# Kernel optimization log

Hardware: AMD Instinct MI355X
Metric: run time of the kernel (lower is better)

## Reference

```python
import jax, jax.numpy as jnp
import numpy as np

B, S, D, H = 2, 2048, 1024, 16
DK = D // H

def setup_inputs() -> dict:
    key = jax.random.key(0)
    ks = jax.random.split(key, 11)
    s = 1.0 / np.sqrt(D)
    return {
        "q": jax.random.normal(ks[0], (B, S, D), jnp.float32),
        "k": jax.random.normal(ks[1], (B, S, D), jnp.float32),
        "v": jax.random.normal(ks[2], (B, S, D), jnp.float32),
        "Wq": jax.random.normal(ks[3], (D, D), jnp.float32) * s,
        "bq": jax.random.normal(ks[4], (D,), jnp.float32) * s,
        "Wk": jax.random.normal(ks[5], (D, D), jnp.float32) * s,
        "bk": jax.random.normal(ks[6], (D,), jnp.float32) * s,
        "Wv": jax.random.normal(ks[7], (D, D), jnp.float32) * s,
        "bv": jax.random.normal(ks[8], (D,), jnp.float32) * s,
        "Wo": jax.random.normal(ks[9], (D, D), jnp.float32) * s,
        "bo": jax.random.normal(ks[10], (D,), jnp.float32) * s,
    }

def reference(q, k, v, Wq, bq, Wk, bk, Wv, bv, Wo, bo):
    # Linear projections, then split into heads: [B,S,D] -> [B,H,S,DK]
    def heads(x, W, b):
        y = x @ W.T + b
        return y.reshape(B, S, H, DK).transpose(0, 2, 1, 3)
    qh = heads(q, Wq, bq)
    kh = heads(k, Wk, bk)
    vh = heads(v, Wv, bv)
    scores = jnp.einsum('bhsd,bhtd->bhst', qh, kh) / jnp.sqrt(jnp.float32(DK))
    attn = jax.nn.softmax(scores, axis=-1)
    out = jnp.einsum('bhst,bhtd->bhsd', attn, vh)  # [B,H,S,DK]
    out = out.transpose(0, 2, 1, 3).reshape(B, S, D)
    return out @ Wo.T + bo
```

## Files before the change

kernel.cpp:

```cpp
#include <hip/hip_runtime.h>
#include <stdint.h>

#define B_  2
#define S_  2048
#define D_  1024
#define H_  16
#define DK_ 64

typedef unsigned short u16;
typedef __attribute__((ext_vector_type(8))) __bf16 bf16x8;
typedef __attribute__((ext_vector_type(4))) float f32x4;
typedef __attribute__((ext_vector_type(16))) float f32x16;
typedef __attribute__((ext_vector_type(4))) short short4v;
typedef __attribute__((ext_vector_type(8))) short short8v;

static __device__ __forceinline__ u16 f2bf(float f) {
    union { float f; uint32_t u; } v; v.f = f;
    return (u16)((v.u + 0x7fffu + ((v.u >> 16) & 1u)) >> 16);
}
static __device__ __forceinline__ uint32_t pk2bf(float x, float y) {
    return (uint32_t)f2bf(x) | ((uint32_t)f2bf(y) << 16);
}
static __device__ __forceinline__ uint32_t cvtpk_bf16(float lo, float hi) {
    uint32_t r; asm("v_cvt_pk_bf16_f32 %0, %1, %2" : "=v"(r) : "v"(lo), "v"(hi));
    return r;
}
static __device__ __forceinline__ float exp2f_fast(float x) {
    float r; asm("v_exp_f32 %0, %1" : "=v"(r) : "v"(x)); return r;
}

#define GLOAD16(gp, lp) \
    __builtin_amdgcn_global_load_lds((const __attribute__((address_space(1))) void*)(gp), \
                                     (__attribute__((address_space(3))) void*)(lp), 16, 0, 0)

static __device__ __forceinline__ int swz(int lin) { return lin ^ ((lin >> 3) & 7); }

static __device__ __forceinline__ int xcd_swz(int bid, int cpx) {
    return (bid & 7) * cpx + (bid >> 3);
}

__global__ __launch_bounds__(256) void cast_all_kernel(
        const float* __restrict__ q, const float* __restrict__ k, const float* __restrict__ v,
        const float* __restrict__ Wq, const float* __restrict__ Wk,
        const float* __restrict__ Wv, const float* __restrict__ Wo,
        u16* __restrict__ qb, u16* __restrict__ kb, u16* __restrict__ vb,
        u16* __restrict__ Wqb, u16* __restrict__ Wkb, u16* __restrict__ Wvb,
        u16* __restrict__ Wob) {
    int blk = blockIdx.x;
    const float* src; u16* dst; int off;
    if (blk < 2048)      { src = q;  dst = qb;  off = blk; }
    else if (blk < 4096) { src = k;  dst = kb;  off = blk - 2048; }
    else if (blk < 6144) { src = v;  dst = vb;  off = blk - 4096; }
    else if (blk < 6656) { src = Wq; dst = Wqb; off = blk - 6144; }
    else if (blk < 7168) { src = Wk; dst = Wkb; off = blk - 6656; }
    else if (blk < 7680) { src = Wv; dst = Wvb; off = blk - 7168; }
    else                 { src = Wo; dst = Wob; off = blk - 7680; }
    int i = (off * 256 + threadIdx.x) * 8;
    float4 a = *(const float4*)(src + i);
    float4 b = *(const float4*)(src + i + 4);
    uint4 r;
    r.x = pk2bf(a.x, a.y); r.y = pk2bf(a.z, a.w);
    r.z = pk2bf(b.x, b.y); r.w = pk2bf(b.z, b.w);
    *(uint4*)(void*)(dst + i) = r;
}

__device__ __forceinline__ void gemm128_compute(
        const u16* __restrict__ X, const u16* __restrict__ W,
        int m0, int n0, u16* lds, f32x4 acc[4][4]) {
    const int tid = threadIdx.x, lane = tid & 63, w = tid >> 6;
    const int wm = w >> 1, wn = w & 1;
    u16* As = lds;
    u16* Bs = lds + 8192;

    auto stage = [&](int bi, int kt) {
#pragma unroll
        for (int r = 0; r < 2; ++r) {
            int s = tid + (r << 8);
            int lin = s ^ ((s >> 3) & 7);
            int row = lin >> 2, ch = lin & 3;
            GLOAD16(X + (size_t)(m0 + row) * 1024 + (kt << 5) + (ch << 3),
                    (char*)(As + bi * 4096) + ((r << 8) + (w << 6)) * 16);
            GLOAD16(W + (size_t)(n0 + row) * 1024 + (kt << 5) + (ch << 3),
                    (char*)(Bs + bi * 4096) + ((r << 8) + (w << 6)) * 16);
        }
    };

    stage(0, 0);
    asm volatile("s_waitcnt vmcnt(0)" ::: "memory");
    __syncthreads();
#pragma unroll 1
    for (int kt = 0; kt < 32; ++kt) {
        const int cur = kt & 1;
        if (kt < 31) stage(cur ^ 1, kt + 1);
        const char* Ab = (const char*)(As + cur * 4096);
        const char* Bb = (const char*)(Bs + cur * 4096);
        bf16x8 a[4], b[4];
#pragma unroll
        for (int f = 0; f < 4; ++f) {
            int rowa = wm * 64 + f * 16 + (lane & 15);
            a[f] = *(const bf16x8*)(Ab + swz(rowa * 4 + (lane >> 4)) * 16);
            int rowb = wn * 64 + f * 16 + (lane & 15);
            b[f] = *(const bf16x8*)(Bb + swz(rowb * 4 + (lane >> 4)) * 16);
        }
#pragma unroll
        for (int fm = 0; fm < 4; ++fm)
#pragma unroll
            for (int fn = 0; fn < 4; ++fn)
                acc[fm][fn] = __builtin_amdgcn_mfma_f32_16x16x32_bf16(
                    a[fm], b[fn], acc[fm][fn], 0, 0, 0);
        __syncthreads();
    }
}

__device__ __forceinline__ void stage_half(const u16* __restrict__ src,
        int R0, int kt, u16* dst, int tid) {
#pragma unroll
    for (int r = 0; r < 2; ++r) {
        int s = tid + (r << 9);
        int lin = s ^ ((s >> 3) & 7);
        int row = lin >> 3, ch = lin & 7;
        GLOAD16(src + (size_t)(R0 + row) * 1024 + (kt << 6) + (ch << 3),
                (char*)dst + ((r << 9) + ((tid >> 6) << 6)) * 16);
    }
}

#define VM4  asm volatile("s_waitcnt vmcnt(4)" ::: "memory")
#define VM0  asm volatile("s_waitcnt vmcnt(0)" ::: "memory")

#define PHASE(QQ, MP, LOADB, STAGE_STMT, VM_STMT)                                \
    {                                                                            \
        bf16x8 afr[2][2];                                                        \
        if (LOADB) {                                                             \
            _Pragma("unroll") for (int fn = 0; fn < 4; ++fn)                     \
            _Pragma("unroll") for (int ks = 0; ks < 2; ++ks) {                   \
                int lin = (brow0 + fn * 16 + (lane & 15)) * 8 + ks * 4 + (lane >> 4); \
                bfr[fn][ks] = *(const bf16x8*)(Bhb[QQ] + swz(lin) * 16);         \
            }                                                                    \
        }                                                                        \
        _Pragma("unroll") for (int fo = 0; fo < 2; ++fo)                         \
        _Pragma("unroll") for (int ks = 0; ks < 2; ++ks) {                       \
            int lin = ((MP) * 32 + fo * 16 + (lane & 15)) * 8 + ks * 4 + (lane >> 4); \
            afr[fo][ks] = *(const bf16x8*)(Ahb[QQ] + swz(lin) * 16);             \
        }                                                                        \
        STAGE_STMT;                                                              \
        VM_STMT;                                                                 \
        __builtin_amdgcn_s_barrier();                                            \
        __builtin_amdgcn_sched_barrier(0);                                       \
        __builtin_amdgcn_s_setprio(1);                                           \
        _Pragma("unroll") for (int fo = 0; fo < 2; ++fo)                         \
        _Pragma("unroll") for (int ks = 0; ks < 2; ++ks)                         \
        _Pragma("unroll") for (int fn = 0; fn < 4; ++fn)                         \
            acc[(MP) * 2 + fo][fn] = __builtin_amdgcn_mfma_f32_16x16x32_bf16(    \
                afr[fo][ks], bfr[fn][ks], acc[(MP) * 2 + fo][fn], 0, 0, 0);      \
        __builtin_amdgcn_s_setprio(0);                                           \
        __builtin_amdgcn_s_barrier();                                            \
        __builtin_amdgcn_sched_barrier(0);                                       \
    }

__global__ __launch_bounds__(512, 2) void qkv256_kernel(
        const u16* __restrict__ qX, const u16* __restrict__ kX, const u16* __restrict__ vX,
        const u16* __restrict__ Wq, const u16* __restrict__ Wk, const u16* __restrict__ Wv,
        const float* __restrict__ bq, const float* __restrict__ bk, const float* __restrict__ bv,
        u16* __restrict__ qo, u16* __restrict__ ko, u16* __restrict__ vt) {
    __shared__ __align__(16) u16 lds[65536];
    const int tid = threadIdx.x, lane = tid & 63, w = tid >> 6;
    const int wm = w >> 2, wn = w & 3;
    const int lg = xcd_swz(blockIdx.x, 24);
    const int which = lg >> 6;
    const int rem = lg & 63;
    const int n0 = (rem >> 4) << 8;
    const int m0 = (rem & 15) << 8;
    const u16* X = which == 0 ? qX : (which == 1 ? kX : vX);
    const u16* W = which == 0 ? Wq : (which == 1 ? Wk : Wv);
    const float* bias = which == 0 ? bq : (which == 1 ? bk : bv);

    u16* Abase = lds;
    u16* Bbase = lds + 32768;

    stage_half(X, m0,        0, Abase + 0,             tid);
    stage_half(X, m0 + 128,  0, Abase + 8192,          tid);
    stage_half(W, n0,        0, Bbase + 0,             tid);
    stage_half(W, n0 + 128,  0, Bbase + 8192,          tid);
    stage_half(W, n0,        1, Bbase + 16384,         tid);
    stage_half(W, n0 + 128,  1, Bbase + 16384 + 8192,  tid);
    VM4;
    __builtin_amdgcn_s_barrier();
    __builtin_amdgcn_sched_barrier(0);

    f32x4 acc[8][4] = {};
    bf16x8 bfr[4][2];
    const char* Ahb[2] = { (const char*)(Abase + wm * 8192),
                           (const char*)(Abase + 16384 + wm * 8192) };
    const char* Bhb[2] = { (const char*)(Bbase + (wn >> 1) * 8192),
                           (const char*)(Bbase + 16384 + (wn >> 1) * 8192) };
    const int brow0 = (wn & 1) * 64;

#pragma unroll 1
    for (int i = 0; i < 8; ++i) {
        const int t0 = 2 * i, t1 = 2 * i + 1;
        const bool nl = (i < 7);
        PHASE(0, 0, true,  stage_half(X, m0,       t1,     Abase + 16384,        tid), (void)0);
        PHASE(0, 1, false, stage_half(X, m0 + 128, t1,     Abase + 16384 + 8192, tid), (void)0);
        PHASE(0, 2, false, if (nl) stage_half(W, n0,       t0 + 2, Bbase + 0,    tid), (void)0);
        PHASE(0, 3, false, if (nl) stage_half(W, n0 + 128, t0 + 2, Bbase + 8192, tid),
              if (nl) { VM4; } else { VM0; });
        PHASE(1, 0, true,  if (nl) stage_half(X, m0,       t0 + 2, Abase + 0,    tid), (void)0);
        PHASE(1, 1, false, if (nl) stage_half(X, m0 + 128, t0 + 2, Abase + 8192, tid), (void)0);
        PHASE(1, 2, false, if (nl) stage_half(W, n0,       t1 + 2, Bbase + 16384, tid), (void)0);
        PHASE(1, 3, false, if (nl) stage_half(W, n0 + 128, t1 + 2, Bbase + 16384 + 8192, tid),
              if (nl) { VM4; });
    }

    if (which < 2) {
        u16* out = which == 0 ? qo : ko;
        const float scale = which == 0 ? 0.1803368801111883f : 1.0f;
#pragma unroll
        for (int fn = 0; fn < 4; ++fn) {
            int n = n0 + wn * 64 + fn * 16 + (lane & 15);
            float bb = bias[n];
            int h = n >> 6, dk = n & 63;
#pragma unroll
            for (int fm = 0; fm < 8; ++fm)
#pragma unroll
                for (int j = 0; j < 4; ++j) {
                    int m = m0 + wm * 128 + fm * 16 + (lane >> 4) * 4 + j;
                    int b = m >> 11, s = m & 2047;
                    out[((size_t)(b * H_ + h) * S_ + s) * DK_ + dk] =
                        f2bf((acc[fm][fn][j] + bb) * scale);
                }
        }
    } else {
        __syncthreads();
        u16* wl = lds + w * 8192;
#pragma unroll
        for (int fn = 0; fn < 4; ++fn) {
            int dk = fn * 16 + (lane & 15);
            float bb = bias[n0 + wn * 64 + dk];
            int xr = (dk & 7) << 3;
#pragma unroll
            for (int fm = 0; fm < 8; ++fm) {
                int sl = fm * 16 + (lane >> 4) * 4;
                short4v p;
#pragma unroll
                for (int j = 0; j < 4; ++j) p[j] = (short)f2bf(acc[fm][fn][j] + bb);
                *(short4v*)(void*)&wl[dk * 128 + (sl ^ xr)] = p;
            }
        }
        int mrow = m0 + wm * 128;
        int b = mrow >> 11, sbase = mrow & 2047;
        int h = (n0 >> 6) + wn;
        u16* dst = vt + ((size_t)(b * H_ + h) * DK_) * S_ + sbase;
#pragma unroll
        for (int oc = 0; oc < 8; ++oc)
#pragma unroll
            for (int ic = 0; ic < 2; ++ic) {
                int dk = oc * 8 + (lane >> 3);
                int sc = ic * 8 + (lane & 7);
                short8v vv = *(const short8v*)(const void*)
                    &wl[dk * 128 + ((sc * 8) ^ ((dk & 7) << 3))];
                *(short8v*)(void*)(dst + (size_t)dk * S_ + sc * 8) = vv;
            }
    }
}

__global__ __launch_bounds__(256) void oproj_kernel(
        const u16* __restrict__ X, const u16* __restrict__ W,
        const float* __restrict__ bias, float* __restrict__ out) {
    __shared__ __align__(16) u16 lds[16384];
    const int bid = xcd_swz(blockIdx.x, 32);
    const int m0 = (bid >> 3) << 7;
    const int n0 = (bid & 7) << 7;
    f32x4 acc[4][4] = {};
    gemm128_compute(X, W, m0, n0, lds, acc);

    const int lane = threadIdx.x & 63, w = threadIdx.x >> 6;
    const int wm = w >> 1, wn = w & 1;
#pragma unroll
    for (int fn = 0; fn < 4; ++fn) {
        int n = n0 + wn * 64 + fn * 16 + (lane & 15);
        float bb = bias[n];
#pragma unroll
        for (int fm = 0; fm < 4; ++fm)
#pragma unroll
            for (int j = 0; j < 4; ++j) {
                int m = m0 + wm * 64 + fm * 16 + (lane >> 4) * 4 + j;
                out[(size_t)m * 1024 + n] = acc[fm][fn][j] + bb;
            }
    }
}

__global__ __launch_bounds__(256, 2) void attn_kernel(
        const u16* __restrict__ qh, const u16* __restrict__ kh,
        const u16* __restrict__ Vt, u16* __restrict__ ao) {
    __shared__ __align__(16) u16 Qs[8192];
    __shared__ __align__(16) u16 Ks[2][4096];
    __shared__ __align__(16) u16 Vs[2][4096];

    const int tid = threadIdx.x, lane = tid & 63, w = tid >> 6;
    const int l31 = lane & 31, hh = lane >> 5;
    const int lg = xcd_swz(blockIdx.x, 64);
    const int bh = lg >> 4, qt = lg & 15;
    const u16* qg = qh + ((size_t)bh * S_ + qt * 128) * DK_;
    const u16* kg = kh + (size_t)bh * S_ * DK_;
    const u16* vg = Vt + (size_t)bh * DK_ * S_;

    auto stageKV = [&](int bi, int kt) {
#pragma unroll
        for (int r = 0; r < 2; ++r) {
            int s = tid + (r << 8);
            int lin = s ^ ((s >> 3) & 7);
            int row = lin >> 3, ch = lin & 7;
            GLOAD16(kg + (size_t)(kt * 64 + row) * 64 + (ch << 3),
                    (char*)(&Ks[bi][0]) + ((r << 8) + (w << 6)) * 16);
            GLOAD16(vg + (size_t)row * S_ + kt * 64 + (ch << 3),
                    (char*)(&Vs[bi][0]) + ((r << 8) + (w << 6)) * 16);
        }
    };

#pragma unroll
    for (int r = 0; r < 4; ++r) {
        int s = tid + (r << 8);
        int lin = s ^ ((s >> 3) & 7);
        int row = lin >> 3, ch = lin & 7;
        GLOAD16(qg + row * 64 + (ch << 3), (char*)Qs + ((r << 8) + (w << 6)) * 16);
    }
    stageKV(0, 0);
    asm volatile("s_waitcnt vmcnt(0)" ::: "memory");
    __syncthreads();

    bf16x8 qf[4];
#pragma unroll
    for (int c = 0; c < 4; ++c) {
        int row = w * 32 + l31;
        qf[c] = *(const bf16x8*)((const char*)Qs + swz(row * 8 + c * 2 + hh) * 16);
    }

    union { short8v s; bf16x8 b; } onesu;
#pragma unroll
    for (int i = 0; i < 8; ++i) onesu.s[i] = 0x3F80;
    const bf16x8 onesf = onesu.b;

    f32x16 acc[2] = {};
    f32x16 accl = {};

#pragma unroll 1
    for (int kt = 0; kt < 32; ++kt) {
        const int cur = kt & 1;
        if (kt < 31) stageKV(cur ^ 1, kt + 1);
        const char* Kb = (const char*)&Ks[cur][0];
        const char* Vb = (const char*)&Vs[cur][0];

        f32x16 st[2] = {};
#pragma unroll
        for (int kb = 0; kb < 2; ++kb) {
            bf16x8 kf[4];
#pragma unroll
            for (int c = 0; c < 4; ++c) {
                int row = kb * 32 + l31;
                kf[c] = *(const bf16x8*)(Kb + swz(row * 8 + c * 2 + hh) * 16);
            }
            __builtin_amdgcn_s_setprio(1);
#pragma unroll
            for (int c = 0; c < 4; ++c)
                st[kb] = __builtin_amdgcn_mfma_f32_32x32x16_bf16(
                    kf[c], qf[c], st[kb], 0, 0, 0);
            __builtin_amdgcn_s_setprio(0);
        }

        bf16x8 pa[4];
#pragma unroll
        for (int c = 0; c < 4; ++c) {
            const int kb = c >> 1, o = (c & 1) * 8;
            float e0 = exp2f_fast(st[kb][o + 0]);
            float e1 = exp2f_fast(st[kb][o + 1]);
            float e2 = exp2f_fast(st[kb][o + 2]);
            float e3 = exp2f_fast(st[kb][o + 3]);
            float e4 = exp2f_fast(st[kb][o + 4]);
            float e5 = exp2f_fast(st[kb][o + 5]);
            float e6 = exp2f_fast(st[kb][o + 6]);
            float e7 = exp2f_fast(st[kb][o + 7]);
            uint32_t u0 = cvtpk_bf16(e0, e1);
            uint32_t u1 = cvtpk_bf16(e2, e3);
            uint32_t u2 = cvtpk_bf16(e4, e5);
            uint32_t u3 = cvtpk_bf16(e6, e7);
            asm volatile("v_permlane32_swap_b32 %0, %1" : "+v"(u0), "+v"(u2));
            asm volatile("v_permlane32_swap_b32 %0, %1" : "+v"(u1), "+v"(u3));
            union { uint32_t u[4]; bf16x8 v; } pu;
            pu.u[0] = u0; pu.u[1] = u1; pu.u[2] = u2; pu.u[3] = u3;
            pa[c] = pu.v;
        }

        __builtin_amdgcn_s_setprio(1);
#pragma unroll
        for (int c = 0; c < 4; ++c)
            accl = __builtin_amdgcn_mfma_f32_32x32x16_bf16(
                pa[c], onesf, accl, 0, 0, 0);
        __builtin_amdgcn_s_setprio(0);
#pragma unroll
        for (int nb = 0; nb < 2; ++nb) {
            bf16x8 vf[4];
#pragma unroll
            for (int c = 0; c < 4; ++c) {
                int row = nb * 32 + l31;
                vf[c] = *(const bf16x8*)(Vb + swz(row * 8 + c * 2 + hh) * 16);
            }
            __builtin_amdgcn_s_setprio(1);
#pragma unroll
            for (int c = 0; c < 4; ++c)
                acc[nb] = __builtin_amdgcn_mfma_f32_32x32x16_bf16(
                    pa[c], vf[c], acc[nb], 0, 0, 0);
            __builtin_amdgcn_s_setprio(0);
        }
        __syncthreads();
    }

    const int bb = bh >> 4, hd = bh & 15;
#pragma unroll
    for (int r = 0; r < 16; ++r) {
        float inv = 1.0f / accl[r];
        int ql = (r & 3) + 8 * (r >> 2) + 4 * hh;
        int srow = qt * 128 + w * 32 + ql;
#pragma unroll
        for (int nb = 0; nb < 2; ++nb) {
            int col = hd * 64 + nb * 32 + l31;
            ao[((size_t)bb * S_ + srow) * D_ + col] = f2bf(acc[nb][r] * inv);
        }
    }
}

extern "C" void kernel_launch(void* const* d_in, const int* in_sizes, int n_in,
                              void* d_out, int out_size, void* d_ws, size_t ws_size,
                              hipStream_t stream) {
    const float* q  = (const float*)d_in[0];
    const float* k  = (const float*)d_in[1];
    const float* v  = (const float*)d_in[2];
    const float* Wq = (const float*)d_in[3];
    const float* bq = (const float*)d_in[4];
    const float* Wk = (const float*)d_in[5];
    const float* bk = (const float*)d_in[6];
    const float* Wv = (const float*)d_in[7];
    const float* bv = (const float*)d_in[8];
    const float* Wo = (const float*)d_in[9];
    const float* bo = (const float*)d_in[10];

    char* ws = (char*)d_ws;
    u16* qb  = (u16*)(ws);
    u16* kb  = (u16*)(ws + (8u  << 20));
    u16* vb  = (u16*)(ws + (16u << 20));
    u16* Wqb = (u16*)(ws + (24u << 20));
    u16* Wkb = (u16*)(ws + (26u << 20));
    u16* Wvb = (u16*)(ws + (28u << 20));
    u16* Wob = (u16*)(ws + (30u << 20));
    u16* qhb = (u16*)(ws + (32u << 20));
    u16* khb = (u16*)(ws + (40u << 20));
    u16* Vtb = (u16*)(ws + (48u << 20));
    u16* aob = kb;

    cast_all_kernel<<<8192, 256, 0, stream>>>(q, k, v, Wq, Wk, Wv, Wo,
                                              qb, kb, vb, Wqb, Wkb, Wvb, Wob);

    qkv256_kernel<<<192, 512, 0, stream>>>(
        qb, kb, vb, Wqb, Wkb, Wvb, bq, bk, bv, qhb, khb, Vtb);

    attn_kernel<<<512, 256, 0, stream>>>(qhb, khb, Vtb, aob);

    oproj_kernel<<<256, 256, 0, stream>>>(aob, Wob, bo, (float*)d_out);
}
```

Baseline: 117.1 us.

## Process two KV tiles per barrier with 4-slot staging and VALU rowsum

The attention loop now handles two 64-key tiles per iteration, using a 4-slot LDS ring that prefetches two tiles ahead, so barriers are halved. The softmax denominator is accumulated with VALU adds and a cross-lane shuffle instead of an extra MFMA against a ones matrix. The swizzle gains an extra XOR term to change LDS bank mapping. LDS use doubles (about 80KB per block), which may reduce occupancy relative to the launch bound of 2 blocks per CU.

```diff
diff --git a/kernel.cpp b/kernel.cpp
--- a/kernel.cpp
+++ b/kernel.cpp
@@ -34,6 +34,9 @@
                                      (__attribute__((address_space(3))) void*)(lp), 16, 0, 0)
 
 static __device__ __forceinline__ int swz(int lin) { return lin ^ ((lin >> 3) & 7); }
+static __device__ __forceinline__ int swz2(int lin) {
+    return lin ^ ((lin >> 3) & 7) ^ ((lin >> 6) & 3);
+}
 
 static __device__ __forceinline__ int xcd_swz(int bid, int cpx) {
     return (bid & 7) * cpx + (bid >> 3);
@@ -293,8 +296,8 @@
         const u16* __restrict__ qh, const u16* __restrict__ kh,
         const u16* __restrict__ Vt, u16* __restrict__ ao) {
     __shared__ __align__(16) u16 Qs[8192];
-    __shared__ __align__(16) u16 Ks[2][4096];
-    __shared__ __align__(16) u16 Vs[2][4096];
+    __shared__ __align__(16) u16 Ks[4][4096];
+    __shared__ __align__(16) u16 Vs[4][4096];
 
     const int tid = threadIdx.x, lane = tid & 63, w = tid >> 6;
     const int l31 = lane & 31, hh = lane >> 5;
@@ -304,27 +307,28 @@
     const u16* kg = kh + (size_t)bh * S_ * DK_;
     const u16* vg = Vt + (size_t)bh * DK_ * S_;
 
-    auto stageKV = [&](int bi, int kt) {
+    auto stageKV = [&](int slot, int kt) {
 #pragma unroll
         for (int r = 0; r < 2; ++r) {
             int s = tid + (r << 8);
-            int lin = s ^ ((s >> 3) & 7);
+            int lin = swz2(s);
             int row = lin >> 3, ch = lin & 7;
             GLOAD16(kg + (size_t)(kt * 64 + row) * 64 + (ch << 3),
-                    (char*)(&Ks[bi][0]) + ((r << 8) + (w << 6)) * 16);
+                    (char*)(&Ks[slot][0]) + ((r << 8) + (w << 6)) * 16);
             GLOAD16(vg + (size_t)row * S_ + kt * 64 + (ch << 3),
-                    (char*)(&Vs[bi][0]) + ((r << 8) + (w << 6)) * 16);
+                    (char*)(&Vs[slot][0]) + ((r << 8) + (w << 6)) * 16);
         }
     };
 
 #pragma unroll
     for (int r = 0; r < 4; ++r) {
         int s = tid + (r << 8);
-        int lin = s ^ ((s >> 3) & 7);
+        int lin = swz2(s);
         int row = lin >> 3, ch = lin & 7;
         GLOAD16(qg + row * 64 + (ch << 3), (char*)Qs + ((r << 8) + (w << 6)) * 16);
     }
     stageKV(0, 0);
+    stageKV(1, 1);
     asm volatile("s_waitcnt vmcnt(0)" ::: "memory");
     __syncthreads();
 
@@ -332,93 +336,84 @@
 #pragma unroll
     for (int c = 0; c < 4; ++c) {
         int row = w * 32 + l31;
-        qf[c] = *(const bf16x8*)((const char*)Qs + swz(row * 8 + c * 2 + hh) * 16);
-    }
-
-    union { short8v s; bf16x8 b; } onesu;
-#pragma unroll
-    for (int i = 0; i < 8; ++i) onesu.s[i] = 0x3F80;
-    const bf16x8 onesf = onesu.b;
+        qf[c] = *(const bf16x8*)((const char*)Qs + swz2(row * 8 + c * 2 + hh) * 16);
+    }
 
     f32x16 acc[2] = {};
-    f32x16 accl = {};
+    float rs = 0.f;
+
+#define ATTN_TILE(SLOT, PAOUT)                                                   \
+    {                                                                            \
+        const char* Kb = (const char*)&Ks[SLOT][0];                              \
+        f32x16 st[2] = {};                                                       \
+        _Pragma("unroll") for (int kb = 0; kb < 2; ++kb) {                       \
+            bf16x8 kf[4];                                                        \
+            _Pragma("unroll") for (int c = 0; c < 4; ++c) {                      \
+                int row = kb * 32 + l31;                                         \
+                kf[c] = *(const bf16x8*)(Kb + swz2(row * 8 + c * 2 + hh) * 16);  \
+            }                                                                    \
+            __builtin_amdgcn_s_setprio(1);                                       \
+            _Pragma("unroll") for (int c = 0; c < 4; ++c)                        \
+                st[kb] = __builtin_amdgcn_mfma_f32_32x32x16_bf16(                \
+                    kf[c], qf[c], st[kb], 0, 0, 0);                              \
+            __builtin_amdgcn_s_setprio(0);                                       \
+        }                                                                        \
+        _Pragma("unroll") for (int c = 0; c < 4; ++c) {                          \
+            const int kb = c >> 1, o = (c & 1) * 8;                              \
+            float e0 = exp2f_fast(st[kb][o + 0]);                                \
+            float e1 = exp2f_fast(st[kb][o + 1]);                                \
+            float e2 = exp2f_fast(st[kb][o + 2]);                                \
+            float e3 = exp2f_fast(st[kb][o + 3]);                                \
+            float e4 = exp2f_fast(st[kb][o + 4]);                                \
+            float e5 = exp2f_fast(st[kb][o + 5]);                                \
+            float e6 = exp2f_fast(st[kb][o + 6]);                                \
+            float e7 = exp2f_fast(st[kb][o + 7]);                                \
+            rs += ((e0 + e1) + (e2 + e3)) + ((e4 + e5) + (e6 + e7));             \
+            uint32_t u0 = cvtpk_bf16(e0, e1);                                    \
+            uint32_t u1 = cvtpk_bf16(e2, e3);                                    \
+            uint32_t u2 = cvtpk_bf16(e4, e5);                                    \
+            uint32_t u3 = cvtpk_bf16(e6, e7);                                    \
+            asm volatile("v_permlane32_swap_b32 %0, %1" : "+v"(u0), "+v"(u2));   \
+            asm volatile("v_permlane32_swap_b32 %0, %1" : "+v"(u1), "+v"(u3));   \
+            union { uint32_t u[4]; bf16x8 v; } pu;                               \
+            pu.u[0] = u0; pu.u[1] = u1; pu.u[2] = u2; pu.u[3] = u3;              \
+            PAOUT[c] = pu.v;                                                     \
+        }                                                                        \
+        const char* Vb = (const char*)&Vs[SLOT][0];                              \
+        _Pragma("unroll") for (int nb = 0; nb < 2; ++nb) {                       \
+            bf16x8 vf[4];                                                        \
+            _Pragma("unroll") for (int c = 0; c < 4; ++c) {                      \
+                int row = nb * 32 + l31;                                         \
+                vf[c] = *(const bf16x8*)(Vb + swz2(row * 8 + c * 2 + hh) * 16);  \
+            }                                                                    \
+            __builtin_amdgcn_s_setprio(1);                                       \
+            _Pragma("unroll") for (int c = 0; c < 4; ++c)                        \
+                acc[nb] = __builtin_amdgcn_mfma_f32_32x32x16_bf16(               \
+                    PAOUT[c], vf[c], acc[nb], 0, 0, 0);                          \
+            __builtin_amdgcn_s_setprio(0);                                       \
+        }                                                                        \
+    }
 
 #pragma unroll 1
-    for (int kt = 0; kt < 32; ++kt) {
-        const int cur = kt & 1;
-        if (kt < 31) stageKV(cur ^ 1, kt + 1);
-        const char* Kb = (const char*)&Ks[cur][0];
-        const char* Vb = (const char*)&Vs[cur][0];
-
-        f32x16 st[2] = {};
-#pragma unroll
-        for (int kb = 0; kb < 2; ++kb) {
-            bf16x8 kf[4];
-#pragma unroll
-            for (int c = 0; c < 4; ++c) {
-                int row = kb * 32 + l31;
-                kf[c] = *(const bf16x8*)(Kb + swz(row * 8 + c * 2 + hh) * 16);
-            }
-            __builtin_amdgcn_s_setprio(1);
-#pragma unroll
-            for (int c = 0; c < 4; ++c)
-                st[kb] = __builtin_amdgcn_mfma_f32_32x32x16_bf16(
-                    kf[c], qf[c], st[kb], 0, 0, 0);
-            __builtin_amdgcn_s_setprio(0);
-        }
-
-        bf16x8 pa[4];
-#pragma unroll
-        for (int c = 0; c < 4; ++c) {
-            const int kb = c >> 1, o = (c & 1) * 8;
-            float e0 = exp2f_fast(st[kb][o + 0]);
-            float e1 = exp2f_fast(st[kb][o + 1]);
-            float e2 = exp2f_fast(st[kb][o + 2]);
-            float e3 = exp2f_fast(st[kb][o + 3]);
-            float e4 = exp2f_fast(st[kb][o + 4]);
-            float e5 = exp2f_fast(st[kb][o + 5]);
-            float e6 = exp2f_fast(st[kb][o + 6]);
-            float e7 = exp2f_fast(st[kb][o + 7]);
-            uint32_t u0 = cvtpk_bf16(e0, e1);
-            uint32_t u1 = cvtpk_bf16(e2, e3);
-            uint32_t u2 = cvtpk_bf16(e4, e5);
-            uint32_t u3 = cvtpk_bf16(e6, e7);
-            asm volatile("v_permlane32_swap_b32 %0, %1" : "+v"(u0), "+v"(u2));
-            asm volatile("v_permlane32_swap_b32 %0, %1" : "+v"(u1), "+v"(u3));
-            union { uint32_t u[4]; bf16x8 v; } pu;
-            pu.u[0] = u0; pu.u[1] = u1; pu.u[2] = u2; pu.u[3] = u3;
-            pa[c] = pu.v;
-        }
-
-        __builtin_amdgcn_s_setprio(1);
-#pragma unroll
-        for (int c = 0; c < 4; ++c)
-            accl = __builtin_amdgcn_mfma_f32_32x32x16_bf16(
-                pa[c], onesf, accl, 0, 0, 0);
-        __builtin_amdgcn_s_setprio(0);
-#pragma unroll
-        for (int nb = 0; nb < 2; ++nb) {
-            bf16x8 vf[4];
-#pragma unroll
-            for (int c = 0; c < 4; ++c) {
-                int row = nb * 32 + l31;
-                vf[c] = *(const bf16x8*)(Vb + swz(row * 8 + c * 2 + hh) * 16);
-            }
-            __builtin_amdgcn_s_setprio(1);
-#pragma unroll
-            for (int c = 0; c < 4; ++c)
-                acc[nb] = __builtin_amdgcn_mfma_f32_32x32x16_bf16(
-                    pa[c], vf[c], acc[nb], 0, 0, 0);
-            __builtin_amdgcn_s_setprio(0);
-        }
+    for (int i = 0; i < 16; ++i) {
+        const int t = 2 * i;
+        if (i < 15) {
+            stageKV((t + 2) & 3, t + 2);
+            stageKV((t + 3) & 3, t + 3);
+        }
+        bf16x8 pa0[4], pa1[4];
+        ATTN_TILE((t) & 3, pa0);
+        ATTN_TILE((t + 1) & 3, pa1);
         __syncthreads();
     }
-
+#undef ATTN_TILE
+
+    rs += __shfl_xor(rs, 32);
     const int bb = bh >> 4, hd = bh & 15;
 #pragma unroll
     for (int r = 0; r < 16; ++r) {
-        float inv = 1.0f / accl[r];
         int ql = (r & 3) + 8 * (r >> 2) + 4 * hh;
+        float inv = 1.0f / __shfl(rs, ql);
         int srow = qt * 128 + w * 32 + ql;
 #pragma unroll
         for (int nb = 0; nb < 2; ++nb) {
```

Result: no change. 115.4 us (-1.5%).

## Double attention query tile per block with 4-stage KV ring and VALU row sums

Applied to the files above, without the earlier changes.

Each attention block now handles 256 query rows (64 per wave, two 32-row sub-tiles), so every K/V tile loaded into LDS feeds twice as many MFMAs, and the grid is halved to 256 blocks. K/V staging becomes a 4-slot ring with prefetch distance 2, using precomputed swizzled source and LDS offsets and a new swizzle. Q is loaded straight from global into registers instead of through LDS. The softmax denominator moves from an MFMA against a ones vector to VALU sums plus shuffles. Higher register pressure drops occupancy to one block per CU, and 256 blocks may underfill the GPU.

```diff
diff --git a/kernel.cpp b/kernel.cpp
--- a/kernel.cpp
+++ b/kernel.cpp
@@ -34,6 +34,9 @@
                                      (__attribute__((address_space(3))) void*)(lp), 16, 0, 0)
 
 static __device__ __forceinline__ int swz(int lin) { return lin ^ ((lin >> 3) & 7); }
+static __device__ __forceinline__ int swz2(int lin) {
+    return lin ^ ((lin >> 3) & 7) ^ ((lin >> 6) & 3);
+}
 
 static __device__ __forceinline__ int xcd_swz(int bid, int cpx) {
     return (bid & 7) * cpx + (bid >> 3);
@@ -289,143 +292,143 @@
     }
 }
 
-__global__ __launch_bounds__(256, 2) void attn_kernel(
+__global__ __launch_bounds__(256, 1) void attn_kernel(
         const u16* __restrict__ qh, const u16* __restrict__ kh,
         const u16* __restrict__ Vt, u16* __restrict__ ao) {
-    __shared__ __align__(16) u16 Qs[8192];
-    __shared__ __align__(16) u16 Ks[2][4096];
-    __shared__ __align__(16) u16 Vs[2][4096];
+    __shared__ __align__(16) u16 Ks[4][4096];
+    __shared__ __align__(16) u16 Vs[4][4096];
 
     const int tid = threadIdx.x, lane = tid & 63, w = tid >> 6;
     const int l31 = lane & 31, hh = lane >> 5;
-    const int lg = xcd_swz(blockIdx.x, 64);
-    const int bh = lg >> 4, qt = lg & 15;
-    const u16* qg = qh + ((size_t)bh * S_ + qt * 128) * DK_;
+    const int lg = xcd_swz(blockIdx.x, 32);
+    const int bh = lg >> 3, qt = lg & 7;
+    const u16* qg = qh + ((size_t)bh * S_ + qt * 256) * DK_;
     const u16* kg = kh + (size_t)bh * S_ * DK_;
     const u16* vg = Vt + (size_t)bh * DK_ * S_;
 
-    auto stageKV = [&](int bi, int kt) {
-#pragma unroll
-        for (int r = 0; r < 2; ++r) {
-            int s = tid + (r << 8);
-            int lin = s ^ ((s >> 3) & 7);
-            int row = lin >> 3, ch = lin & 7;
-            GLOAD16(kg + (size_t)(kt * 64 + row) * 64 + (ch << 3),
-                    (char*)(&Ks[bi][0]) + ((r << 8) + (w << 6)) * 16);
-            GLOAD16(vg + (size_t)row * S_ + kt * 64 + (ch << 3),
-                    (char*)(&Vs[bi][0]) + ((r << 8) + (w << 6)) * 16);
-        }
+    const int lin0 = swz2(tid), lin1 = swz2(tid + 256);
+    const u16* ksrc0 = kg + (lin0 >> 3) * 64 + ((lin0 & 7) << 3);
+    const u16* ksrc1 = kg + (lin1 >> 3) * 64 + ((lin1 & 7) << 3);
+    const u16* vsrc0 = vg + (size_t)(lin0 >> 3) * S_ + ((lin0 & 7) << 3);
+    const u16* vsrc1 = vg + (size_t)(lin1 >> 3) * S_ + ((lin1 & 7) << 3);
+    char* kdst0 = (char*)(&Ks[0][0]) + (w << 6) * 16;
+    char* kdst1 = (char*)(&Ks[0][0]) + (256 + (w << 6)) * 16;
+    char* vdst0 = (char*)(&Vs[0][0]) + (w << 6) * 16;
+    char* vdst1 = (char*)(&Vs[0][0]) + (256 + (w << 6)) * 16;
+
+    auto stageKV = [&](int slot, int kt) {
+        const int sb = slot << 13;
+        GLOAD16(ksrc0 + (kt << 12), kdst0 + sb);
+        GLOAD16(ksrc1 + (kt << 12), kdst1 + sb);
+        GLOAD16(vsrc0 + (kt << 6),  vdst0 + sb);
+        GLOAD16(vsrc1 + (kt << 6),  vdst1 + sb);
     };
 
-#pragma unroll
-    for (int r = 0; r < 4; ++r) {
-        int s = tid + (r << 8);
-        int lin = s ^ ((s >> 3) & 7);
-        int row = lin >> 3, ch = lin & 7;
-        GLOAD16(qg + row * 64 + (ch << 3), (char*)Qs + ((r << 8) + (w << 6)) * 16);
-    }
+    int loff[2][4];
+#pragma unroll
+    for (int b = 0; b < 2; ++b)
+#pragma unroll
+        for (int c = 0; c < 4; ++c)
+            loff[b][c] = swz2((b * 32 + l31) * 8 + c * 2 + hh) * 16;
+
     stageKV(0, 0);
+    stageKV(1, 1);
+    bf16x8 qf[2][4];
+#pragma unroll
+    for (int qb = 0; qb < 2; ++qb)
+#pragma unroll
+        for (int c = 0; c < 4; ++c)
+            qf[qb][c] = *(const bf16x8*)(qg +
+                (size_t)(w * 64 + qb * 32 + l31) * 64 + c * 16 + hh * 8);
     asm volatile("s_waitcnt vmcnt(0)" ::: "memory");
     __syncthreads();
 
-    bf16x8 qf[4];
-#pragma unroll
-    for (int c = 0; c < 4; ++c) {
-        int row = w * 32 + l31;
-        qf[c] = *(const bf16x8*)((const char*)Qs + swz(row * 8 + c * 2 + hh) * 16);
-    }
-
-    union { short8v s; bf16x8 b; } onesu;
-#pragma unroll
-    for (int i = 0; i < 8; ++i) onesu.s[i] = 0x3F80;
-    const bf16x8 onesf = onesu.b;
-
-    f32x16 acc[2] = {};
-    f32x16 accl = {};
+    f32x16 acc[2][2] = {};
+    float rs[2] = {0.f, 0.f};
 
 #pragma unroll 1
-    for (int kt = 0; kt < 32; ++kt) {
-        const int cur = kt & 1;
-        if (kt < 31) stageKV(cur ^ 1, kt + 1);
-        const char* Kb = (const char*)&Ks[cur][0];
-        const char* Vb = (const char*)&Vs[cur][0];
-
-        f32x16 st[2] = {};
+    for (int i = 0; i < 32; ++i) {
+        if (i < 30) stageKV((i + 2) & 3, i + 2);
+
+        const char* Kb = (const char*)(&Ks[0][0]) + ((i & 3) << 13);
+        f32x16 st[2][2] = {};
 #pragma unroll
         for (int kb = 0; kb < 2; ++kb) {
             bf16x8 kf[4];
 #pragma unroll
+            for (int c = 0; c < 4; ++c)
+                kf[c] = *(const bf16x8*)(Kb + loff[kb][c]);
+            __builtin_amdgcn_s_setprio(1);
+#pragma unroll
+            for (int qb = 0; qb < 2; ++qb)
+#pragma unroll
+                for (int c = 0; c < 4; ++c)
+                    st[qb][kb] = __builtin_amdgcn_mfma_f32_32x32x16_bf16(
+                        kf[c], qf[qb][c], st[qb][kb], 0, 0, 0);
+            __builtin_amdgcn_s_setprio(0);
+        }
+
+        bf16x8 pa[2][4];
+#pragma unroll
+        for (int qb = 0; qb < 2; ++qb)
+#pragma unroll
             for (int c = 0; c < 4; ++c) {
-                int row = kb * 32 + l31;
-                kf[c] = *(const bf16x8*)(Kb + swz(row * 8 + c * 2 + hh) * 16);
+                const int kb = c >> 1, o = (c & 1) * 8;
+                float e0 = exp2f_fast(st[qb][kb][o + 0]);
+                float e1 = exp2f_fast(st[qb][kb][o + 1]);
+                float e2 = exp2f_fast(st[qb][kb][o + 2]);
+                float e3 = exp2f_fast(st[qb][kb][o + 3]);
+                float e4 = exp2f_fast(st[qb][kb][o + 4]);
+                float e5 = exp2f_fast(st[qb][kb][o + 5]);
+                float e6 = exp2f_fast(st[qb][kb][o + 6]);
+                float e7 = exp2f_fast(st[qb][kb][o + 7]);
+                rs[qb] += ((e0 + e1) + (e2 + e3)) + ((e4 + e5) + (e6 + e7));
+                uint32_t u0 = cvtpk_bf16(e0, e1);
+                uint32_t u1 = cvtpk_bf16(e2, e3);
+                uint32_t u2 = cvtpk_bf16(e4, e5);
+                uint32_t u3 = cvtpk_bf16(e6, e7);
+                asm volatile("v_permlane32_swap_b32 %0, %1" : "+v"(u0), "+v"(u2));
+                asm volatile("v_permlane32_swap_b32 %0, %1" : "+v"(u1), "+v"(u3));
+                union { uint32_t u[4]; bf16x8 v; } pu;
+                pu.u[0] = u0; pu.u[1] = u1; pu.u[2] = u2; pu.u[3] = u3;
+                pa[qb][c] = pu.v;
             }
-            __builtin_amdgcn_s_setprio(1);
-#pragma unroll
-            for (int c = 0; c < 4; ++c)
-                st[kb] = __builtin_amdgcn_mfma_f32_32x32x16_bf16(
-                    kf[c], qf[c], st[kb], 0, 0, 0);
-            __builtin_amdgcn_s_setprio(0);
-        }
-
-        bf16x8 pa[4];
-#pragma unroll
-        for (int c = 0; c < 4; ++c) {
-            const int kb = c >> 1, o = (c & 1) * 8;
-            float e0 = exp2f_fast(st[kb][o + 0]);
-            float e1 = exp2f_fast(st[kb][o + 1]);
-            float e2 = exp2f_fast(st[kb][o + 2]);
-            float e3 = exp2f_fast(st[kb][o + 3]);
-            float e4 = exp2f_fast(st[kb][o + 4]);
-            float e5 = exp2f_fast(st[kb][o + 5]);
-            float e6 = exp2f_fast(st[kb][o + 6]);
-            float e7 = exp2f_fast(st[kb][o + 7]);
-            uint32_t u0 = cvtpk_bf16(e0, e1);
-            uint32_t u1 = cvtpk_bf16(e2, e3);
-            uint32_t u2 = cvtpk_bf16(e4, e5);
-            uint32_t u3 = cvtpk_bf16(e6, e7);
-            asm volatile("v_permlane32_swap_b32 %0, %1" : "+v"(u0), "+v"(u2));
-            asm volatile("v_permlane32_swap_b32 %0, %1" : "+v"(u1), "+v"(u3));
-            union { uint32_t u[4]; bf16x8 v; } pu;
-            pu.u[0] = u0; pu.u[1] = u1; pu.u[2] = u2; pu.u[3] = u3;
-            pa[c] = pu.v;
-        }
-
-        __builtin_amdgcn_s_setprio(1);
-#pragma unroll
-        for (int c = 0; c < 4; ++c)
-            accl = __builtin_amdgcn_mfma_f32_32x32x16_bf16(
-                pa[c], onesf, accl, 0, 0, 0);
-        __builtin_amdgcn_s_setprio(0);
+
+        const char* Vb = (const char*)(&Vs[0][0]) + ((i & 3) << 13);
 #pragma unroll
         for (int nb = 0; nb < 2; ++nb) {
             bf16x8 vf[4];
 #pragma unroll
-            for (int c = 0; c < 4; ++c) {
-                int row = nb * 32 + l31;
-                vf[c] = *(const bf16x8*)(Vb + swz(row * 8 + c * 2 + hh) * 16);
+            for (int c = 0; c < 4; ++c)
+                vf[c] = *(const bf16x8*)(Vb + loff[nb][c]);
+            __builtin_amdgcn_s_setprio(1);
+#pragma unroll
+            for (int qb = 0; qb < 2; ++qb)
+#pragma unroll
+                for (int c = 0; c < 4; ++c)
+                    acc[qb][nb] = __builtin_amdgcn_mfma_f32_32x32x16_bf16(
+                        pa[qb][c], vf[c], acc[qb][nb], 0, 0, 0);
+            __builtin_amdgcn_s_setprio(0);
+        }
+        __syncthreads();
+    }
+
+    rs[0] += __shfl_xor(rs[0], 32);
+    rs[1] += __shfl_xor(rs[1], 32);
+    const int bb = bh >> 4, hd = bh & 15;
+#pragma unroll
+    for (int qb = 0; qb < 2; ++qb)
+#pragma unroll
+        for (int r = 0; r < 16; ++r) {
+            int ql = (r & 3) + 8 * (r >> 2) + 4 * hh;
+            float inv = 1.0f / __shfl(rs[qb], ql);
+            int srow = qt * 256 + w * 64 + qb * 32 + ql;
+#pragma unroll
+            for (int nb = 0; nb < 2; ++nb) {
+                int col = hd * 64 + nb * 32 + l31;
+                ao[((size_t)bb * S_ + srow) * D_ + col] = f2bf(acc[qb][nb][r] * inv);
             }
-            __builtin_amdgcn_s_setprio(1);
-#pragma unroll
-            for (int c = 0; c < 4; ++c)
-                acc[nb] = __builtin_amdgcn_mfma_f32_32x32x16_bf16(
-                    pa[c], vf[c], acc[nb], 0, 0, 0);
-            __builtin_amdgcn_s_setprio(0);
-        }
-        __syncthreads();
-    }
-
-    const int bb = bh >> 4, hd = bh & 15;
-#pragma unroll
-    for (int r = 0; r < 16; ++r) {
-        float inv = 1.0f / accl[r];
-        int ql = (r & 3) + 8 * (r >> 2) + 4 * hh;
-        int srow = qt * 128 + w * 32 + ql;
-#pragma unroll
-        for (int nb = 0; nb < 2; ++nb) {
-            int col = hd * 64 + nb * 32 + l31;
-            ao[((size_t)bb * S_ + srow) * D_ + col] = f2bf(acc[nb][r] * inv);
-        }
-    }
+        }
 }
 
 extern "C" void kernel_launch(void* const* d_in, const int* in_sizes, int n_in,
@@ -462,7 +465,7 @@
     qkv256_kernel<<<192, 512, 0, stream>>>(
         qb, kb, vb, Wqb, Wkb, Wvb, bq, bk, bv, qhb, khb, Vtb);
 
-    attn_kernel<<<512, 256, 0, stream>>>(qhb, khb, Vtb, aob);
+    attn_kernel<<<256, 256, 0, stream>>>(qhb, khb, Vtb, aob);
 
     oproj_kernel<<<256, 256, 0, stream>>>(aob, Wob, bo, (float*)d_out);
 }
```

New measurement: 135.5 us. +15.7%, slower.
